# Kernel tuning notes

Measured on AMD Instinct MI355X. Metric: run time of the kernel, lower is better.

## Reference

```python
import jax, jax.numpy as jnp
import numpy as np
from itertools import product

D = 96  # input grid resolution; after subdivision it is 2*D = 192
N_VOX = 20000
C_IN = 64
C_OUT = 64

OFFSETS = jnp.array(list(product([-1, 0, 1], repeat=3)), dtype=jnp.int32)   # [27,3] conv neighborhood
CHILD = jnp.array(list(product([0, 1], repeat=3)), dtype=jnp.int32)        # [8,3] subdivision children


def _lin(coords, d):
    # linearize (z,y,x)-style coords into a flat index for the dense lookup grid
    return (coords[:, 0] * d + coords[:, 1]) * d + coords[:, 2]


def _submanifold_conv3d(coords, feats, W, b, d):
    """Submanifold sparse 3x3x3 conv: output only at active sites.
    coords: [N,3] int32, feats: [N,Cin], W: [27,Cin,Cout], b: [Cout]."""
    n = coords.shape[0]
    grid = jnp.full((d * d * d,), -1, dtype=jnp.int32).at[_lin(coords, d)].set(
        jnp.arange(n, dtype=jnp.int32))
    out = jnp.broadcast_to(b, (n, b.shape[0])).astype(feats.dtype)
    for k in range(27):  # fixed small kernel loop (unrolled under jit)
        nb = coords + OFFSETS[k]
        inb = jnp.all((nb >= 0) & (nb < d), axis=1)
        idx = grid[_lin(jnp.clip(nb, 0, d - 1), d)]
        mask = (inb & (idx >= 0)).astype(feats.dtype)
        f = feats[jnp.maximum(idx, 0)] * mask[:, None]  # gather active neighbors
        out = out + f @ W[k]
    return out


def setup_inputs() -> dict:
    rng = np.random.default_rng(0)
    lin = rng.choice(D ** 3, size=N_VOX, replace=False)  # unique active voxels
    coords = np.stack([lin // (D * D), (lin // D) % D, lin % D], axis=1).astype(np.int32)
    key = jax.random.key(0)
    k1, k2, k3, k4, k5 = jax.random.split(key, 5)
    scale = 1.0 / np.sqrt(27.0 * C_IN)
    return {
        "coords": jnp.asarray(coords),
        "feats": jax.random.normal(k1, (N_VOX, C_IN), jnp.float32),
        "W1": jax.random.normal(k2, (27, C_IN, C_OUT), jnp.float32) * scale,
        "b1": jax.random.normal(k3, (C_OUT,), jnp.float32) * 0.01,
        "W2": jax.random.normal(k4, (27, C_OUT, C_OUT), jnp.float32) * scale,
        "b2": jax.random.normal(k5, (C_OUT,), jnp.float32) * 0.01,
    }


def reference(coords, feats, W1, b1, W2, b2):
    # act_layers: SparseConv3d + SiLU
    h = jax.nn.silu(_submanifold_conv3d(coords, feats, W1, b1, D))
    n = coords.shape[0]
    coords2 = ((coords * 2)[:, None, :] + CHILD[None, :, :]).reshape(8 * n, 3)
    h2 = jnp.repeat(h, 8, axis=0)  # matches (N,8,C)->(8N,C) child order
    # out_layers: SparseConv3d + SiLU at doubled resolution
    return jax.nn.silu(_submanifold_conv3d(coords2, h2, W2, b2, 2 * D))
```

## Files before the change

kernel.cpp:

```cpp
#include <hip/hip_runtime.h>

#define D1 96
#define GRID_VOX (D1 * D1 * D1)
#define CAP2S 8
#define OS 68

typedef __attribute__((ext_vector_type(8))) short short8_t;
typedef __attribute__((ext_vector_type(4))) float f32x4;

__device__ __forceinline__ unsigned short bf16rne(float x) {
    unsigned u = __float_as_uint(x);
    return (unsigned short)((u + 0x7FFF + ((u >> 16) & 1)) >> 16);
}
__device__ __forceinline__ void split2(float v, unsigned short& hi,
                                       unsigned short& lo) {
    hi = bf16rne(v);
    float hf = __uint_as_float((unsigned)hi << 16);
    lo = bf16rne(v - hf);
}
__device__ __forceinline__ float silu(float v) {
    return v / (1.f + __expf(-v));
}

__global__ void setupA_kernel(const float* __restrict__ W1,
                              const int* __restrict__ coords,
                              unsigned short* __restrict__ grid,
                              unsigned short* __restrict__ Wpk1h,
                              unsigned short* __restrict__ Wpk1l, int n) {
    int t = blockIdx.x * blockDim.x + threadIdx.x;
    if (t < 512) {
        int fid = t >> 6, l = t & 63;
        int kb = fid >> 2, c = fid & 3;
#pragma unroll
        for (int e = 0; e < 8; ++e) {
            int ci = kb * 32 + ((l >> 4) << 3) + e;
            int co = c * 16 + (l & 15);
            unsigned short hi, lo;
            split2(W1[13 * 4096 + ci * 64 + co], hi, lo);
            Wpk1h[(size_t)t * 8 + e] = hi;
            Wpk1l[(size_t)t * 8 + e] = lo;
        }
    } else {
        int i = t - 512;
        if (i < n)
            grid[(coords[3 * i] * D1 + coords[3 * i + 1]) * D1 +
                 coords[3 * i + 2]] = (unsigned short)(i + 1);
    }
}

__device__ __forceinline__ void load_split_A(const float* __restrict__ src,
                                             int arow, int lane, short8_t& ah0,
                                             short8_t& al0, short8_t& ah1,
                                             short8_t& al1) {
    const float* ap = src + (size_t)arow * 64 + ((lane >> 4) << 3);
    f32x4 a0 = *(const f32x4*)(ap);
    f32x4 a1 = *(const f32x4*)(ap + 4);
    f32x4 a2 = *(const f32x4*)(ap + 32);
    f32x4 a3 = *(const f32x4*)(ap + 36);
#pragma unroll
    for (int e = 0; e < 4; ++e) {
        unsigned short hh, ll;
        split2(a0[e], hh, ll); ah0[e] = (short)hh; al0[e] = (short)ll;
        split2(a1[e], hh, ll); ah0[4 + e] = (short)hh; al0[4 + e] = (short)ll;
        split2(a2[e], hh, ll); ah1[e] = (short)hh; al1[e] = (short)ll;
        split2(a3[e], hh, ll); ah1[4 + e] = (short)hh; al1[4 + e] = (short)ll;
    }
}

__device__ __forceinline__ void dense_mfma8(const short8_t ah0, const short8_t al0,
                                            const short8_t ah1, const short8_t al1,
                                            const short8_t* __restrict__ Bh,
                                            const short8_t* __restrict__ Bl,
                                            const float* __restrict__ bias,
                                            float* __restrict__ oT, int w,
                                            int lane) {
    int c0 = (w >> 2) * 2;
#pragma unroll
    for (int cc = 0; cc < 2; ++cc) {
        int c = c0 + cc;
        short8_t bh0 = Bh[c * 64 + lane];
        short8_t bl0 = Bl[c * 64 + lane];
        short8_t bh1 = Bh[(4 + c) * 64 + lane];
        short8_t bl1 = Bl[(4 + c) * 64 + lane];
        f32x4 acc = {0.f, 0.f, 0.f, 0.f};
        acc = __builtin_amdgcn_mfma_f32_16x16x32_bf16(ah0, bh0, acc, 0, 0, 0);
        acc = __builtin_amdgcn_mfma_f32_16x16x32_bf16(al0, bh0, acc, 0, 0, 0);
        acc = __builtin_amdgcn_mfma_f32_16x16x32_bf16(ah0, bl0, acc, 0, 0, 0);
        acc = __builtin_amdgcn_mfma_f32_16x16x32_bf16(ah1, bh1, acc, 0, 0, 0);
        acc = __builtin_amdgcn_mfma_f32_16x16x32_bf16(al1, bh1, acc, 0, 0, 0);
        acc = __builtin_amdgcn_mfma_f32_16x16x32_bf16(ah1, bl1, acc, 0, 0, 0);
        int col = c * 16 + (lane & 15);
        float bb = bias[col];
#pragma unroll
        for (int r = 0; r < 4; ++r) {
            int row = (w & 3) * 16 + ((lane >> 4) << 2) + r;
            oT[row * OS + col] = acc[r] + bb;
        }
    }
}

__device__ __forceinline__ void scan64(int cnt, int lane, int* pfxs, int* cnts,
                                       int* nps) {
    int val = cnt;
#pragma unroll
    for (int off = 1; off < 64; off <<= 1) {
        int v2 = __shfl_up(val, off);
        if (lane >= off) val += v2;
    }
    pfxs[lane] = val - cnt;
    cnts[lane] = cnt;
    if (lane == 63) nps[0] = val;
}

__device__ __forceinline__ void fixup_loop(const float* __restrict__ src,
                                           const float* __restrict__ Wbase,
                                           const int* __restrict__ pl, int np,
                                           float fsc[8][2][64],
                                           float* __restrict__ oT, int w,
                                           int lane) {
    int it = 0;
#pragma unroll 1
    for (int p = w; p < np; p += 8, ++it) {
        int e = pl[p];
        int j = e & 0x1FFFF, tag = (e >> 17) & 31, row = (e >> 23) & 63;
        float fv = src[(size_t)j * 64 + lane];
        int buf = it & 1;
        fsc[w][buf][lane] = fv;
        const float* wk = Wbase + (size_t)tag * 4096;
        float a0 = 0.f, a1 = 0.f, a2 = 0.f, a3 = 0.f;
#pragma unroll
        for (int c4 = 0; c4 < 16; ++c4) {
            f32x4 fb = *(f32x4*)&fsc[w][buf][c4 * 4];
            a0 += fb[0] * wk[(c4 * 4 + 0) * 64 + lane];
            a1 += fb[1] * wk[(c4 * 4 + 1) * 64 + lane];
            a2 += fb[2] * wk[(c4 * 4 + 2) * 64 + lane];
            a3 += fb[3] * wk[(c4 * 4 + 3) * 64 + lane];
        }
        atomicAdd(&oT[row * OS + lane], (a0 + a1) + (a2 + a3));
    }
}

__global__ __launch_bounds__(512) void conv1_fused_kernel(
    const int* __restrict__ coords, const float* __restrict__ feats,
    const float* __restrict__ W1, const float* __restrict__ W2,
    const unsigned short* __restrict__ Wpk1h,
    const unsigned short* __restrict__ Wpk1l, const float* __restrict__ b1,
    const unsigned short* __restrict__ grid, int* __restrict__ c2s,
    int* __restrict__ p2s, unsigned short* __restrict__ Wpk2h,
    unsigned short* __restrict__ Wpk2l, float* __restrict__ W2e,
    float* __restrict__ h, int n, int nblk) {
    if (blockIdx.x >= nblk) {
        int t = (blockIdx.x - nblk) * 512 + threadIdx.x;
        if (t < 4096) {
            int u = t;
            int fid = u >> 6, l = u & 63;
            int s = fid >> 3, kb = (fid >> 2) & 1, c = fid & 3;
            int s0 = (s >> 2) & 1, s1 = (s >> 1) & 1, s2 = s & 1;
#pragma unroll
            for (int e = 0; e < 8; ++e) {
                int ci = kb * 32 + ((l >> 4) << 3) + e;
                int co = c * 16 + (l & 15);
                float sum = 0.f;
                for (int o0 = -s0; o0 <= 1 - s0; ++o0)
                    for (int o1 = -s1; o1 <= 1 - s1; ++o1)
                        for (int o2 = -s2; o2 <= 1 - s2; ++o2) {
                            int k = (o0 + 1) * 9 + (o1 + 1) * 3 + (o2 + 1);
                            sum += W2[k * 4096 + ci * 64 + co];
                        }
                unsigned short hi, lo;
                split2(sum, hi, lo);
                Wpk2h[(size_t)u * 8 + e] = hi;
                Wpk2l[(size_t)u * 8 + e] = lo;
            }
        } else if (t < 4096 + 262144) {
            int r = t - 4096;
            int sd = r >> 12, e = r & 4095;
            int s = sd >> 3, d = sd & 7;
            int sa[3] = { (s >> 2) & 1, (s >> 1) & 1, s & 1 };
            int da[3] = { (d >> 2) & 1, (d >> 1) & 1, d & 1 };
            int lo_[3], hi_[3];
            for (int a = 0; a < 3; ++a) {
                int p = sa[a] - 1 + da[a];
                int l = 2 * p - sa[a];     if (l < -1) l = -1;
                int hh = 2 * p + 1 - sa[a]; if (hh > 1) hh = 1;
                lo_[a] = l; hi_[a] = hh;
            }
            float sum = 0.f;
            for (int o0 = lo_[0]; o0 <= hi_[0]; ++o0)
                for (int o1 = lo_[1]; o1 <= hi_[1]; ++o1)
                    for (int o2 = lo_[2]; o2 <= hi_[2]; ++o2) {
                        int k = (o0 + 1) * 9 + (o1 + 1) * 3 + (o2 + 1);
                        sum += W2[k * 4096 + e];
                    }
            W2e[(size_t)sd * 4096 + e] = sum;
        }
        return;
    }

    __shared__ __align__(16) float oT[64 * OS];
    __shared__ __align__(16) float fsc[8][2][64];
    __shared__ int plt[64 * 26];
    __shared__ int pl[1664];
    __shared__ int pfxs[64], cnts_s[64], nps[1];
    int base = blockIdx.x * 64;
    int t = threadIdx.x, w = t >> 6, lane = t & 63;

    if (t < 64) {
        int myv = base + t;
        int cnt = 0;
        if (myv < n) {
            int c0 = coords[3 * myv], c1v = coords[3 * myv + 1],
                c2v = coords[3 * myv + 2];
            int n2[8] = {0, 0, 0, 0, 0, 0, 0, 0};
#pragma unroll 1
            for (int g = 0; g < 3; ++g) {
                int jv9[9];
                int kb = g * 9;
#pragma unroll
                for (int u = 0; u < 9; ++u) {
                    int k = kb + u;
                    int o0 = k / 9 - 1, o1 = (k / 3) % 3 - 1, o2 = k % 3 - 1;
                    int x0 = c0 + o0, x1 = c1v + o1, x2 = c2v + o2;
                    bool inb = (unsigned)x0 < D1 && (unsigned)x1 < D1 &&
                               (unsigned)x2 < D1;
                    jv9[u] = inb ? (int)grid[(x0 * D1 + x1) * D1 + x2] : 0;
                }
#pragma unroll
                for (int u = 0; u < 9; ++u) {
                    int k = kb + u;
                    if (k == 13) continue;
                    int j1 = jv9[u];
                    if (j1 < 1 || j1 > n) continue;
                    int o0 = k / 9 - 1, o1 = (k / 3) % 3 - 1, o2 = k % 3 - 1;
                    int x0 = c0 + o0, x1 = c1v + o1, x2 = c2v + o2;
                    int jj = j1 - 1;
                    if (coords[3 * jj] != x0 || coords[3 * jj + 1] != x1 ||
                        coords[3 * jj + 2] != x2)
                        continue;
                    plt[t * 26 + cnt] = jj | (k << 17);
                    ++cnt;
#pragma unroll
                    for (int s = 0; s < 8; ++s) {
                        int d0 = o0 + 1 - ((s >> 2) & 1);
                        int d1 = o1 + 1 - ((s >> 1) & 1);
                        int d2 = o2 + 1 - (s & 1);
                        if (((d0 | d1 | d2) & ~1) == 0) {
                            int d = (d0 << 2) | (d1 << 1) | d2;
                            p2s[((size_t)myv * 8 + s) * CAP2S + n2[s]] =
                                jj | (d << 17);
                            ++n2[s];
                        }
                    }
                }
            }
#pragma unroll
            for (int s = 0; s < 8; ++s) c2s[myv * 8 + s] = n2[s];
        }
        scan64(cnt, lane, pfxs, cnts_s, nps);
    }

    int arow = base + (w & 3) * 16 + (lane & 15);
    if (arow >= n) arow = n - 1;
    short8_t ah0, al0, ah1, al1;
    load_split_A(feats, arow, lane, ah0, al0, ah1, al1);
    dense_mfma8(ah0, al0, ah1, al1, (const short8_t*)Wpk1h,
                (const short8_t*)Wpk1l, b1, oT, w, lane);
    __syncthreads();

    {
        int row = t & 63, e0 = t >> 6;
        int cr = cnts_s[row], pf = pfxs[row];
        for (int e = e0; e < cr; e += 8)
            pl[pf + e] = plt[row * 26 + e] | (row << 23);
    }
    __syncthreads();

    fixup_loop(feats, W1, pl, nps[0], fsc, oT, w, lane);
    __syncthreads();

    {
        int r = t >> 3, c8 = (t & 7) * 8;
        if (base + r < n) {
#pragma unroll
            for (int jj = 0; jj < 2; ++jj) {
                f32x4 v = *(f32x4*)&oT[r * OS + c8 + jj * 4];
#pragma unroll
                for (int u = 0; u < 4; ++u) v[u] = silu(v[u]);
                *(f32x4*)&h[(size_t)(base + r) * 64 + c8 + jj * 4] = v;
            }
        }
    }
}

__global__ __launch_bounds__(512) void conv2_fused_kernel(
    const float* __restrict__ h, const unsigned short* __restrict__ Wpk2h,
    const unsigned short* __restrict__ Wpk2l, const float* __restrict__ W2e,
    const float* __restrict__ b2, const int* __restrict__ c2s,
    const int* __restrict__ p2s, float* __restrict__ out, int n) {
    __shared__ __align__(16) float oT[64 * OS];
    __shared__ __align__(16) float fsc[8][2][64];
    __shared__ int pl[448];
    __shared__ int pfxs[64], cnts_s[64], nps[1];
    int idx = blockIdx.x;
    int Tm = idx & 7, s = (idx >> 3) & 7, T = (idx >> 6) * 8 + Tm;
    int base = T * 64;
    if (base >= n) return;
    int t = threadIdx.x, w = t >> 6, lane = t & 63;

    if (t < 64) {
        int cnt = (base + lane < n) ? c2s[(size_t)(base + lane) * 8 + s] : 0;
        scan64(cnt, lane, pfxs, cnts_s, nps);
    }

    int arow = base + (w & 3) * 16 + (lane & 15);
    if (arow >= n) arow = n - 1;
    short8_t ah0, al0, ah1, al1;
    load_split_A(h, arow, lane, ah0, al0, ah1, al1);
    dense_mfma8(ah0, al0, ah1, al1,
                (const short8_t*)Wpk2h + (size_t)s * 8 * 64,
                (const short8_t*)Wpk2l + (size_t)s * 8 * 64, b2, oT, w, lane);
    __syncthreads();

    {
        int row = t & 63, e0 = t >> 6;
        int cr = cnts_s[row], pf = pfxs[row];
        for (int e = e0; e < cr; e += 8)
            pl[pf + e] =
                p2s[((size_t)(base + row) * 8 + s) * CAP2S + e] | (row << 23);
    }
    __syncthreads();

    fixup_loop(h, W2e + (size_t)s * 8 * 4096, pl, nps[0], fsc, oT, w, lane);
    __syncthreads();

    {
        int r = t >> 3, c8 = (t & 7) * 8;
        if (base + r < n) {
#pragma unroll
            for (int jj = 0; jj < 2; ++jj) {
                f32x4 v = *(f32x4*)&oT[r * OS + c8 + jj * 4];
#pragma unroll
                for (int u = 0; u < 4; ++u) v[u] = silu(v[u]);
                *(f32x4*)&out[((size_t)(base + r) * 8 + s) * 64 + c8 + jj * 4] = v;
            }
        }
    }
}

extern "C" void kernel_launch(void* const* d_in, const int* in_sizes, int n_in,
                              void* d_out, int out_size, void* d_ws,
                              size_t ws_size, hipStream_t stream) {
    const int* coords = (const int*)d_in[0];
    const float* feats = (const float*)d_in[1];
    const float* W1 = (const float*)d_in[2];
    const float* b1 = (const float*)d_in[3];
    const float* W2 = (const float*)d_in[4];
    const float* b2 = (const float*)d_in[5];
    float* out = (float*)d_out;

    int n = in_sizes[0] / 3;
    int nblk = (n + 63) / 64;

    char* ws = (char*)d_ws;
    size_t off = 0;
    auto alloc = [&](size_t bytes) {
        size_t o = off;
        off = (off + bytes + 255) & ~(size_t)255;
        return o;
    };
    unsigned short* grid1 = (unsigned short*)(ws + alloc((size_t)GRID_VOX * 2));
    float* h      = (float*)(ws + alloc((size_t)n * 64 * 4));
    float* W2e    = (float*)(ws + alloc(64 * 4096 * 4));
    unsigned short* Wpk1h = (unsigned short*)(ws + alloc(512 * 8 * 2));
    unsigned short* Wpk1l = (unsigned short*)(ws + alloc(512 * 8 * 2));
    unsigned short* Wpk2h = (unsigned short*)(ws + alloc(4096 * 8 * 2));
    unsigned short* Wpk2l = (unsigned short*)(ws + alloc(4096 * 8 * 2));
    int*   c2s    = (int*)(ws + alloc((size_t)n * 8 * 4));
    int*   p2s    = (int*)(ws + alloc((size_t)n * 8 * CAP2S * 4));

    setupA_kernel<<<(512 + n + 255) / 256, 256, 0, stream>>>(
        W1, coords, grid1, Wpk1h, Wpk1l, n);

    int prepBlocks = (4096 + 262144 + 511) / 512;
    conv1_fused_kernel<<<nblk + prepBlocks, 512, 0, stream>>>(
        coords, feats, W1, W2, Wpk1h, Wpk1l, b1, grid1, c2s, p2s, Wpk2h,
        Wpk2l, W2e, h, n, nblk);

    int nTileGrp = (nblk + 7) / 8;
    conv2_fused_kernel<<<nTileGrp * 64, 512, 0, stream>>>(
        h, Wpk2h, Wpk2l, W2e, b2, c2s, p2s, out, n);
}
```

Baseline: 79.53 us.

## Halve conv1 tile to 32 voxels per block to double block count

```diff
diff --git a/kernel.cpp b/kernel.cpp
--- a/kernel.cpp
+++ b/kernel.cpp
@@ -64,6 +64,34 @@
         split2(a1[e], hh, ll); ah0[4 + e] = (short)hh; al0[4 + e] = (short)ll;
         split2(a2[e], hh, ll); ah1[e] = (short)hh; al1[e] = (short)ll;
         split2(a3[e], hh, ll); ah1[4 + e] = (short)hh; al1[4 + e] = (short)ll;
+    }
+}
+
+__device__ __forceinline__ void dense_mfma32(const short8_t ah0, const short8_t al0,
+                                             const short8_t ah1, const short8_t al1,
+                                             const short8_t* __restrict__ Bh,
+                                             const short8_t* __restrict__ Bl,
+                                             const float* __restrict__ bias,
+                                             float* __restrict__ oT, int w,
+                                             int lane) {
+    int c = w >> 1;
+    short8_t bh0 = Bh[c * 64 + lane];
+    short8_t bl0 = Bl[c * 64 + lane];
+    short8_t bh1 = Bh[(4 + c) * 64 + lane];
+    short8_t bl1 = Bl[(4 + c) * 64 + lane];
+    f32x4 acc = {0.f, 0.f, 0.f, 0.f};
+    acc = __builtin_amdgcn_mfma_f32_16x16x32_bf16(ah0, bh0, acc, 0, 0, 0);
+    acc = __builtin_amdgcn_mfma_f32_16x16x32_bf16(al0, bh0, acc, 0, 0, 0);
+    acc = __builtin_amdgcn_mfma_f32_16x16x32_bf16(ah0, bl0, acc, 0, 0, 0);
+    acc = __builtin_amdgcn_mfma_f32_16x16x32_bf16(ah1, bh1, acc, 0, 0, 0);
+    acc = __builtin_amdgcn_mfma_f32_16x16x32_bf16(al1, bh1, acc, 0, 0, 0);
+    acc = __builtin_amdgcn_mfma_f32_16x16x32_bf16(ah1, bl1, acc, 0, 0, 0);
+    int col = c * 16 + (lane & 15);
+    float bb = bias[col];
+#pragma unroll
+    for (int r = 0; r < 4; ++r) {
+        int row = (w & 1) * 16 + ((lane >> 4) << 2) + r;
+        oT[row * OS + col] = acc[r] + bb;
     }
 }
 
@@ -148,9 +176,9 @@
     const unsigned short* __restrict__ grid, int* __restrict__ c2s,
     int* __restrict__ p2s, unsigned short* __restrict__ Wpk2h,
     unsigned short* __restrict__ Wpk2l, float* __restrict__ W2e,
-    float* __restrict__ h, int n, int nblk) {
-    if (blockIdx.x >= nblk) {
-        int t = (blockIdx.x - nblk) * 512 + threadIdx.x;
+    float* __restrict__ h, int n, int nblk1) {
+    if (blockIdx.x >= nblk1) {
+        int t = (blockIdx.x - nblk1) * 512 + threadIdx.x;
         if (t < 4096) {
             int u = t;
             int fid = u >> 6, l = u & 63;
@@ -197,80 +225,85 @@
         return;
     }
 
-    __shared__ __align__(16) float oT[64 * OS];
+    __shared__ __align__(16) float oT[32 * OS];
     __shared__ __align__(16) float fsc[8][2][64];
-    __shared__ int plt[64 * 26];
-    __shared__ int pl[1664];
+    __shared__ int plt[32 * 26];
+    __shared__ int pl[832];
     __shared__ int pfxs[64], cnts_s[64], nps[1];
-    int base = blockIdx.x * 64;
+    int base = blockIdx.x * 32;
     int t = threadIdx.x, w = t >> 6, lane = t & 63;
 
     if (t < 64) {
-        int myv = base + t;
         int cnt = 0;
-        if (myv < n) {
-            int c0 = coords[3 * myv], c1v = coords[3 * myv + 1],
-                c2v = coords[3 * myv + 2];
-            int n2[8] = {0, 0, 0, 0, 0, 0, 0, 0};
+        if (t < 32) {
+            int myv = base + t;
+            if (myv < n) {
+                int c0 = coords[3 * myv], c1v = coords[3 * myv + 1],
+                    c2v = coords[3 * myv + 2];
+                int n2[8] = {0, 0, 0, 0, 0, 0, 0, 0};
 #pragma unroll 1
-            for (int g = 0; g < 3; ++g) {
-                int jv9[9];
-                int kb = g * 9;
-#pragma unroll
-                for (int u = 0; u < 9; ++u) {
-                    int k = kb + u;
-                    int o0 = k / 9 - 1, o1 = (k / 3) % 3 - 1, o2 = k % 3 - 1;
-                    int x0 = c0 + o0, x1 = c1v + o1, x2 = c2v + o2;
-                    bool inb = (unsigned)x0 < D1 && (unsigned)x1 < D1 &&
-                               (unsigned)x2 < D1;
-                    jv9[u] = inb ? (int)grid[(x0 * D1 + x1) * D1 + x2] : 0;
-                }
-#pragma unroll
-                for (int u = 0; u < 9; ++u) {
-                    int k = kb + u;
-                    if (k == 13) continue;
-                    int j1 = jv9[u];
-                    if (j1 < 1 || j1 > n) continue;
-                    int o0 = k / 9 - 1, o1 = (k / 3) % 3 - 1, o2 = k % 3 - 1;
-                    int x0 = c0 + o0, x1 = c1v + o1, x2 = c2v + o2;
-                    int jj = j1 - 1;
-                    if (coords[3 * jj] != x0 || coords[3 * jj + 1] != x1 ||
-                        coords[3 * jj + 2] != x2)
-                        continue;
-                    plt[t * 26 + cnt] = jj | (k << 17);
-                    ++cnt;
-#pragma unroll
-                    for (int s = 0; s < 8; ++s) {
-                        int d0 = o0 + 1 - ((s >> 2) & 1);
-                        int d1 = o1 + 1 - ((s >> 1) & 1);
-                        int d2 = o2 + 1 - (s & 1);
-                        if (((d0 | d1 | d2) & ~1) == 0) {
-                            int d = (d0 << 2) | (d1 << 1) | d2;
-                            p2s[((size_t)myv * 8 + s) * CAP2S + n2[s]] =
-                                jj | (d << 17);
-                            ++n2[s];
+                for (int g = 0; g < 3; ++g) {
+                    int jv9[9];
+                    int kb = g * 9;
+#pragma unroll
+                    for (int u = 0; u < 9; ++u) {
+                        int k = kb + u;
+                        int o0 = k / 9 - 1, o1 = (k / 3) % 3 - 1,
+                            o2 = k % 3 - 1;
+                        int x0 = c0 + o0, x1 = c1v + o1, x2 = c2v + o2;
+                        bool inb = (unsigned)x0 < D1 && (unsigned)x1 < D1 &&
+                                   (unsigned)x2 < D1;
+                        jv9[u] = inb ? (int)grid[(x0 * D1 + x1) * D1 + x2] : 0;
+                    }
+#pragma unroll
+                    for (int u = 0; u < 9; ++u) {
+                        int k = kb + u;
+                        if (k == 13) continue;
+                        int j1 = jv9[u];
+                        if (j1 < 1 || j1 > n) continue;
+                        int o0 = k / 9 - 1, o1 = (k / 3) % 3 - 1,
+                            o2 = k % 3 - 1;
+                        int x0 = c0 + o0, x1 = c1v + o1, x2 = c2v + o2;
+                        int jj = j1 - 1;
+                        if (coords[3 * jj] != x0 ||
+                            coords[3 * jj + 1] != x1 ||
+                            coords[3 * jj + 2] != x2)
+                            continue;
+                        plt[t * 26 + cnt] = jj | (k << 17);
+                        ++cnt;
+#pragma unroll
+                        for (int s = 0; s < 8; ++s) {
+                            int d0 = o0 + 1 - ((s >> 2) & 1);
+                            int d1 = o1 + 1 - ((s >> 1) & 1);
+                            int d2 = o2 + 1 - (s & 1);
+                            if (((d0 | d1 | d2) & ~1) == 0) {
+                                int d = (d0 << 2) | (d1 << 1) | d2;
+                                p2s[((size_t)myv * 8 + s) * CAP2S + n2[s]] =
+                                    jj | (d << 17);
+                                ++n2[s];
+                            }
                         }
                     }
                 }
+#pragma unroll
+                for (int s = 0; s < 8; ++s) c2s[myv * 8 + s] = n2[s];
             }
-#pragma unroll
-            for (int s = 0; s < 8; ++s) c2s[myv * 8 + s] = n2[s];
         }
         scan64(cnt, lane, pfxs, cnts_s, nps);
     }
 
-    int arow = base + (w & 3) * 16 + (lane & 15);
+    int arow = base + (w & 1) * 16 + (lane & 15);
     if (arow >= n) arow = n - 1;
     short8_t ah0, al0, ah1, al1;
     load_split_A(feats, arow, lane, ah0, al0, ah1, al1);
-    dense_mfma8(ah0, al0, ah1, al1, (const short8_t*)Wpk1h,
-                (const short8_t*)Wpk1l, b1, oT, w, lane);
+    dense_mfma32(ah0, al0, ah1, al1, (const short8_t*)Wpk1h,
+                 (const short8_t*)Wpk1l, b1, oT, w, lane);
     __syncthreads();
 
     {
-        int row = t & 63, e0 = t >> 6;
+        int row = t & 31, e0 = t >> 5;
         int cr = cnts_s[row], pf = pfxs[row];
-        for (int e = e0; e < cr; e += 8)
+        for (int e = e0; e < cr; e += 16)
             pl[pf + e] = plt[row * 26 + e] | (row << 23);
     }
     __syncthreads();
@@ -279,15 +312,12 @@
     __syncthreads();
 
     {
-        int r = t >> 3, c8 = (t & 7) * 8;
+        int r = t >> 4, c4 = (t & 15) * 4;
         if (base + r < n) {
-#pragma unroll
-            for (int jj = 0; jj < 2; ++jj) {
-                f32x4 v = *(f32x4*)&oT[r * OS + c8 + jj * 4];
-#pragma unroll
-                for (int u = 0; u < 4; ++u) v[u] = silu(v[u]);
-                *(f32x4*)&h[(size_t)(base + r) * 64 + c8 + jj * 4] = v;
-            }
+            f32x4 v = *(f32x4*)&oT[r * OS + c4];
+#pragma unroll
+            for (int u = 0; u < 4; ++u) v[u] = silu(v[u]);
+            *(f32x4*)&h[(size_t)(base + r) * 64 + c4] = v;
         }
     }
 }
@@ -360,6 +390,7 @@
 
     int n = in_sizes[0] / 3;
     int nblk = (n + 63) / 64;
+    int nblk1 = (n + 31) / 32;
 
     char* ws = (char*)d_ws;
     size_t off = 0;
@@ -382,9 +413,9 @@
         W1, coords, grid1, Wpk1h, Wpk1l, n);
 
     int prepBlocks = (4096 + 262144 + 511) / 512;
-    conv1_fused_kernel<<<nblk + prepBlocks, 512, 0, stream>>>(
+    conv1_fused_kernel<<<nblk1 + prepBlocks, 512, 0, stream>>>(
         coords, feats, W1, W2, Wpk1h, Wpk1l, b1, grid1, c2s, p2s, Wpk2h,
-        Wpk2l, W2e, h, n, nblk);
+        Wpk2l, W2e, h, n, nblk1);
 
     int nTileGrp = (nblk + 7) / 8;
     conv2_fused_kernel<<<nTileGrp * 64, 512, 0, stream>>>(
```

After: 74.41 us. 6.4% less time.
